# Optimization experiments

Measured on AMD Instinct MI355X. Metric: run time of the kernel, lower is better.

## Reference

```python
import jax, jax.numpy as jnp
import numpy as np

EMB = 8
HID = 64
B = 1000
T = 512
N = (B * T) // 5  # events per source; sources partition the (batch,time) grid

_KEYS = ["ccba", "cdtx", "cust", "dp", "remit"]
_NUMS = {"ccba": 8, "cdtx": 1, "cust": 1, "dp": 2, "remit": 1}
_CATS = {"ccba": 0, "cdtx": 2, "cust": 3, "dp": 8, "remit": 1}
_VOCAB = {"ccba": 0, "cdtx": 179, "cust": 37, "dp": 435, "remit": 5}


def setup_inputs() -> dict:
    ks = iter(jax.random.split(jax.random.key(0), 64))
    rng = np.random.default_rng(0)
    chunks = np.split(rng.permutation(B * T), 5)
    d = {}
    for k5, ch in zip(_KEYS, chunks):
        d[k5 + "_num"] = jax.random.normal(next(ks), (N, _NUMS[k5]), jnp.float32)
        if _CATS[k5] > 0:
            d[k5 + "_cat"] = jax.random.randint(next(ks), (N, _CATS[k5]), 0, _VOCAB[k5])
            d[k5 + "_tab"] = jax.random.normal(next(ks), (_VOCAB[k5], EMB), jnp.float32) * 0.1
        d[k5 + "_bi"] = jnp.asarray(ch // T, jnp.int32)
        d[k5 + "_ti"] = jnp.asarray(ch % T, jnp.int32)
        in_dim = _CATS[k5] * EMB + _NUMS[k5]
        d[k5 + "_W"] = jax.random.normal(next(ks), (in_dim, HID), jnp.float32) * np.float32(1.0 / np.sqrt(in_dim))
        d[k5 + "_b"] = jnp.zeros((HID,), jnp.float32)
    # LSTM: 2 layers x 2 directions, hidden 64, proj_size 1 -> layer1 input is 2
    for l, insz in [(0, HID), (1, 2)]:
        d[f"Wih{l}"] = jax.random.normal(next(ks), (2, 4 * HID, insz), jnp.float32) * 0.05
        d[f"Whh{l}"] = jax.random.normal(next(ks), (2, 4 * HID, 1), jnp.float32) * 0.05
        d[f"Whr{l}"] = jax.random.normal(next(ks), (2, 1, HID), jnp.float32) * 0.05
        d[f"bih{l}"] = jnp.zeros((2, 4 * HID), jnp.float32)
        d[f"bhh{l}"] = jnp.zeros((2, 4 * HID), jnp.float32)
    d["length"] = T
    d["batch_size"] = B
    return d


def _embed(num, cat, tab, W, b):
    # FeatureEmbedder: concat(categorical embeddings, numeric) -> Linear(hidden)
    x = num if cat is None else jnp.concatenate([tab[cat].reshape(cat.shape[0], -1), num], axis=-1)
    return x @ W + b


def _lstm_dir(x, Wih, Whh, Whr, bih, bhh, reverse):
    Bx = x.shape[0]
    H = Whr.shape[1]
    p = Whr.shape[0]
    bias = bih + bhh

    def step(carry, xt):
        h, c = carry  # h: [B,p] projected hidden, c: [B,H] cell
        g = xt @ Wih.T + h @ Whh.T + bias
        i, f, gg, o = jnp.split(g, 4, axis=-1)  # PyTorch gate order i,f,g,o
        c = jax.nn.sigmoid(f) * c + jax.nn.sigmoid(i) * jnp.tanh(gg)
        h = (jax.nn.sigmoid(o) * jnp.tanh(c)) @ Whr.T  # proj_size projection
        return (h, c), h

    init = (jnp.zeros((Bx, p), x.dtype), jnp.zeros((Bx, H), x.dtype))
    _, ys = jax.lax.scan(step, init, jnp.swapaxes(x, 0, 1), reverse=reverse)
    return jnp.swapaxes(ys, 0, 1)  # [B,T,p]


def _bilstm(x, Wih, Whh, Whr, bih, bhh):
    fwd = _lstm_dir(x, Wih[0], Whh[0], Whr[0], bih[0], bhh[0], False)
    bwd = _lstm_dir(x, Wih[1], Whh[1], Whr[1], bih[1], bhh[1], True)
    return jnp.concatenate([fwd, bwd], axis=-1)


def _forward(a):
    feat = jnp.zeros((a["batch_size"], a["length"], HID), jnp.float32)
    for k5 in _KEYS:
        v = _embed(a[k5 + "_num"], a.get(k5 + "_cat"), a.get(k5 + "_tab"), a[k5 + "_W"], a[k5 + "_b"])
        feat = feat.at[a[k5 + "_bi"], a[k5 + "_ti"]].set(v)  # scatter-assemble padded tensor
    h = _bilstm(feat, a["Wih0"], a["Whh0"], a["Whr0"], a["bih0"], a["bhh0"])
    h = _bilstm(h, a["Wih1"], a["Whh1"], a["Whr1"], a["bih1"], a["bhh1"])
    return h.mean(axis=2)  # [B,T]


def reference(ccba_num, ccba_bi, ccba_ti, ccba_W, ccba_b,
              cdtx_num, cdtx_cat, cdtx_tab, cdtx_bi, cdtx_ti, cdtx_W, cdtx_b,
              cust_num, cust_cat, cust_tab, cust_bi, cust_ti, cust_W, cust_b,
              dp_num, dp_cat, dp_tab, dp_bi, dp_ti, dp_W, dp_b,
              remit_num, remit_cat, remit_tab, remit_bi, remit_ti, remit_W, remit_b,
              Wih0, Whh0, Whr0, bih0, bhh0, Wih1, Whh1, Whr1, bih1, bhh1,
              length, batch_size):
    return _forward(dict(locals()))
```

## Files before the change

### kernel.cpp

```cpp
#include <hip/hip_runtime.h>
#include <cstdint>
#include <cstddef>

#define TLEN 512
#define BATCH 1000
#define NEVS 102400
#define HID 64
#define W0S 8
#define NP (TLEN / W0S)

__device__ __forceinline__ float fast_rcp(float x) {
#if __has_builtin(__builtin_amdgcn_rcpf)
    return __builtin_amdgcn_rcpf(x);
#else
    return 1.0f / x;
#endif
}
__device__ __forceinline__ float sigm(float x) { return fast_rcp(1.0f + __expf(-x)); }
__device__ __forceinline__ float tanh_f(float x) { return fmaf(2.0f, sigm(2.0f * x), -1.0f); }

__device__ __forceinline__ float wave_sum_bcast(float x) {
#if __has_builtin(__builtin_amdgcn_update_dpp) && __has_builtin(__builtin_amdgcn_readlane)
    x += __int_as_float(__builtin_amdgcn_update_dpp(0, __float_as_int(x), 0x111, 0xf, 0xf, true));
    x += __int_as_float(__builtin_amdgcn_update_dpp(0, __float_as_int(x), 0x112, 0xf, 0xf, true));
    x += __int_as_float(__builtin_amdgcn_update_dpp(0, __float_as_int(x), 0x114, 0xf, 0xf, true));
    x += __int_as_float(__builtin_amdgcn_update_dpp(0, __float_as_int(x), 0x118, 0xf, 0xf, true));
    x += __int_as_float(__builtin_amdgcn_update_dpp(0, __float_as_int(x), 0x142, 0xa, 0xf, true));
    x += __int_as_float(__builtin_amdgcn_update_dpp(0, __float_as_int(x), 0x143, 0xc, 0xf, true));
    return __int_as_float(__builtin_amdgcn_readlane(__float_as_int(x), 63));
#else
#pragma unroll
    for (int off = 1; off < 64; off <<= 1) x += __shfl_xor(x, off, 64);
    return x;
#endif
}

__device__ __forceinline__ void wave_sum2(float& a, float& b) {
#if __has_builtin(__builtin_amdgcn_update_dpp) && __has_builtin(__builtin_amdgcn_readlane)
    int ta, tb;
    ta = __builtin_amdgcn_update_dpp(0, __float_as_int(a), 0x111, 0xf, 0xf, true);
    tb = __builtin_amdgcn_update_dpp(0, __float_as_int(b), 0x111, 0xf, 0xf, true);
    a += __int_as_float(ta); b += __int_as_float(tb);
    ta = __builtin_amdgcn_update_dpp(0, __float_as_int(a), 0x112, 0xf, 0xf, true);
    tb = __builtin_amdgcn_update_dpp(0, __float_as_int(b), 0x112, 0xf, 0xf, true);
    a += __int_as_float(ta); b += __int_as_float(tb);
    ta = __builtin_amdgcn_update_dpp(0, __float_as_int(a), 0x114, 0xf, 0xf, true);
    tb = __builtin_amdgcn_update_dpp(0, __float_as_int(b), 0x114, 0xf, 0xf, true);
    a += __int_as_float(ta); b += __int_as_float(tb);
    ta = __builtin_amdgcn_update_dpp(0, __float_as_int(a), 0x118, 0xf, 0xf, true);
    tb = __builtin_amdgcn_update_dpp(0, __float_as_int(b), 0x118, 0xf, 0xf, true);
    a += __int_as_float(ta); b += __int_as_float(tb);
    ta = __builtin_amdgcn_update_dpp(0, __float_as_int(a), 0x142, 0xa, 0xf, true);
    tb = __builtin_amdgcn_update_dpp(0, __float_as_int(b), 0x142, 0xa, 0xf, true);
    a += __int_as_float(ta); b += __int_as_float(tb);
    ta = __builtin_amdgcn_update_dpp(0, __float_as_int(a), 0x143, 0xc, 0xf, true);
    tb = __builtin_amdgcn_update_dpp(0, __float_as_int(b), 0x143, 0xc, 0xf, true);
    a += __int_as_float(ta); b += __int_as_float(tb);
    a = __int_as_float(__builtin_amdgcn_readlane(__float_as_int(a), 63));
    b = __int_as_float(__builtin_amdgcn_readlane(__float_as_int(b), 63));
#else
    a = wave_sum_bcast(a); b = wave_sum_bcast(b);
#endif
}

__global__ __launch_bounds__(256) void map_build_kernel(
    const int* __restrict__ b0, const int* __restrict__ t0,
    const int* __restrict__ b1, const int* __restrict__ t1,
    const int* __restrict__ b2, const int* __restrict__ t2,
    const int* __restrict__ b3, const int* __restrict__ t3,
    const int* __restrict__ b4, const int* __restrict__ t4,
    int* __restrict__ map)
{
    const int src = blockIdx.y;
    const int* bi = src == 0 ? b0 : src == 1 ? b1 : src == 2 ? b2 : src == 3 ? b3 : b4;
    const int* ti = src == 0 ? t0 : src == 1 ? t1 : src == 2 ? t2 : src == 3 ? t3 : t4;
    const int e = blockIdx.x * 256 + threadIdx.x;
    map[bi[e] * TLEN + ti[e]] = (src << 20) | e;
}

__global__ __launch_bounds__(512) void compose_kernel(
    const float* __restrict__ W0, const float* __restrict__ B0,
    const float* __restrict__ W1, const float* __restrict__ B1,
    const float* __restrict__ W2, const float* __restrict__ B2,
    const float* __restrict__ W3, const float* __restrict__ B3,
    const float* __restrict__ W4, const float* __restrict__ B4,
    const float* __restrict__ Wih, const float* __restrict__ bih,
    const float* __restrict__ bhh, float* __restrict__ wp)
{
    const int col = threadIdx.x;
    const int row = blockIdx.x;
    const float* srcW; const float* srcB; int base, IND;
    if (row < 9)        { srcW = W0; srcB = B0; base = 0;   IND = 8;  }
    else if (row < 27)  { srcW = W1; srcB = B1; base = 9;   IND = 17; }
    else if (row < 53)  { srcW = W2; srcB = B2; base = 27;  IND = 25; }
    else if (row < 120) { srcW = W3; srcB = B3; base = 53;  IND = 66; }
    else                { srcW = W4; srcB = B4; base = 120; IND = 9;  }
    const int j = row - base;
    const float* xrow = (j < IND) ? (srcW + (size_t)j * 64) : srcB;
    const float* wr = Wih + (size_t)col * 64;
    float acc = 0.0f;
#pragma unroll
    for (int h2 = 0; h2 < 64; ++h2) acc = fmaf(xrow[h2], wr[h2], acc);
    if (j == IND) acc += bih[col] + bhh[col];
    wp[(size_t)row * 512 + col] = acc;
}

template<int NB, int BASE>
__device__ __forceinline__ float4 dot4(const float* wT, const float* xb, int colq) {
    float ax = 0.f, ay = 0.f, az = 0.f, aw = 0.f;
#pragma unroll
    for (int jb = 0; jb < NB; ++jb) {
        const float4 x4 = *(const float4*)(xb + 4 * jb);
        const float* w = wT + (size_t)(BASE + 4 * jb) * 256 + 4 * colq;
        const float4 w0 = *(const float4*)(w);
        const float4 w1 = *(const float4*)(w + 256);
        const float4 w2 = *(const float4*)(w + 512);
        const float4 w3 = *(const float4*)(w + 768);
        ax = fmaf(x4.x, w0.x, ax); ay = fmaf(x4.x, w0.y, ay);
        az = fmaf(x4.x, w0.z, az); aw = fmaf(x4.x, w0.w, aw);
        ax = fmaf(x4.y, w1.x, ax); ay = fmaf(x4.y, w1.y, ay);
        az = fmaf(x4.y, w1.z, az); aw = fmaf(x4.y, w1.w, aw);
        ax = fmaf(x4.z, w2.x, ax); ay = fmaf(x4.z, w2.y, ay);
        az = fmaf(x4.z, w2.z, az); aw = fmaf(x4.z, w2.w, aw);
        ax = fmaf(x4.w, w3.x, ax); ay = fmaf(x4.w, w3.y, ay);
        az = fmaf(x4.w, w3.z, az); aw = fmaf(x4.w, w3.w, aw);
    }
    return make_float4(ax, ay, az, aw);
}

__global__ __launch_bounds__(576, 1) void fused0_kernel(
    const float* __restrict__ ccba_num,
    const float* __restrict__ cdtx_num, const int* __restrict__ cdtx_cat, const float* __restrict__ cdtx_tab,
    const float* __restrict__ cust_num, const int* __restrict__ cust_cat, const float* __restrict__ cust_tab,
    const float* __restrict__ dp_num,   const int* __restrict__ dp_cat,   const float* __restrict__ dp_tab,
    const float* __restrict__ remit_num, const int* __restrict__ remit_cat, const float* __restrict__ remit_tab,
    const float* __restrict__ wp, const int* __restrict__ map,
    const float* __restrict__ Whh, const float* __restrict__ Whr,
    float* __restrict__ h0)
{
    __shared__ float wT[132 * 256];
    __shared__ float winP[2][W0S][256];
    __shared__ float xbuf[2][W0S][68];
    __shared__ int   mcls[2][W0S];

    const int tid = threadIdx.x;
    const int b = blockIdx.x >> 1, dir = blockIdx.x & 1;

    {
        const float4* wp4 = (const float4*)wp;
        float4* wT4 = (float4*)wT;
        for (int i = tid; i < 130 * 64; i += 576) {
            const int row = i >> 6, c4 = i & 63;
            wT4[(row << 6) + c4] = wp4[(row << 7) + (dir << 6) + c4];
        }
        if (tid < 128) wT4[130 * 64 + tid] = make_float4(0.f, 0.f, 0.f, 0.f);
    }

    float whh4[4] = {0.f, 0.f, 0.f, 0.f};
    float whr = 0.f, h = 0.f, c = 0.f;
    float* h0p = h0 + (size_t)b * TLEN * 2 + dir;
    if (tid >= 512) {
        const int lane = tid - 512;
#pragma unroll
        for (int k = 0; k < 4; ++k) whh4[k] = Whh[dir * 256 + k * 64 + lane];
        whr = Whr[dir * HID + lane];
    }

    struct GR { float v0, v1; int mc; };

    auto g_load = [&](int P) -> GR {
        GR g; g.v0 = 0.f; g.v1 = 0.f;
        const int ev = tid >> 6, v = tid & 63;
        const int s = P * W0S + ev;
        const int t = dir ? (TLEN - 1 - s) : s;
        g.mc = map[b * TLEN + t];
        const int src = g.mc >> 20, e = g.mc & 0xFFFFF;
        switch (src) {
        case 0:
            g.v0 = (v < 8) ? ccba_num[(size_t)e * 8 + v] : (v == 8 ? 1.0f : 0.0f);
            break;
        case 1:
            g.v0 = (v < 16) ? cdtx_tab[(size_t)cdtx_cat[e * 2 + (v >> 3)] * 8 + (v & 7)]
                 : (v == 16 ? cdtx_num[e] : (v == 17 ? 1.0f : 0.0f));
            break;
        case 2:
            g.v0 = (v < 24) ? cust_tab[(size_t)cust_cat[e * 3 + (v >> 3)] * 8 + (v & 7)]
                 : (v == 24 ? cust_num[e] : (v == 25 ? 1.0f : 0.0f));
            break;
        case 3:
            g.v0 = dp_tab[(size_t)dp_cat[e * 8 + (v >> 3)] * 8 + (v & 7)];
            if (v < 4) g.v1 = (v < 2) ? dp_num[(size_t)e * 2 + v] : (v == 2 ? 1.0f : 0.0f);
            break;
        default:
            g.v0 = (v < 8) ? remit_tab[(size_t)remit_cat[e] * 8 + v]
                 : (v == 8 ? remit_num[e] : (v == 9 ? 1.0f : 0.0f));
            break;
        }
        return g;
    };
    auto g_store = [&](const GR& g, int P) {
        const int buf = P & 1;
        const int ev = tid >> 6, v = tid & 63;
        if (v == 0) mcls[buf][ev] = g.mc;
        const int src = g.mc >> 20;
        const int pad = (src == 0) ? 12 : (src == 1) ? 20 : (src == 2) ? 28
                      : (src == 3) ? 64 : 12;
        if (v < pad) xbuf[buf][ev][v] = g.v0;
        if (src == 3 && v < 4) xbuf[buf][ev][64 + v] = g.v1;
    };

    auto a1 = [&](int P) {
        const int buf = P & 1;
        const int ev = tid >> 6, colq = tid & 63;
        const int src = mcls[buf][ev] >> 20;
        const float* xb = xbuf[buf][ev];
        float4 acc;
        switch (src) {
        case 0:  acc = dot4<3, 0>(wT, xb, colq);   break;
        case 1:  acc = dot4<5, 9>(wT, xb, colq);   break;
        case 2:  acc = dot4<7, 27>(wT, xb, colq);  break;
        case 3:  acc = dot4<17, 53>(wT, xb, colq); break;
        default: acc = dot4<3, 120>(wT, xb, colq); break;
        }
        ((float4*)winP[buf][ev])[colq] = acc;
    };

    auto bstep = [&](int P) {
        const int buf = P & 1;
        const int lane = tid - 512;
        for (int sl = 0; sl < W0S; ++sl) {
            const float gi = fmaf(whh4[0], h, winP[buf][sl][lane]);
            const float gf = fmaf(whh4[1], h, winP[buf][sl][64 + lane]);
            const float gg = fmaf(whh4[2], h, winP[buf][sl][128 + lane]);
            const float go = fmaf(whh4[3], h, winP[buf][sl][192 + lane]);
            c = sigm(gf) * c + sigm(gi) * tanh_f(gg);
            h = wave_sum_bcast(sigm(go) * tanh_f(c) * whr);
            const int s = P * W0S + sl;
            const int tt = dir ? (TLEN - 1 - s) : s;
            if (lane == 0) h0p[(size_t)tt * 2] = h;
        }
    };

    if (tid < 512) { GR g0 = g_load(0); g_store(g0, 0); }
    __syncthreads();
    if (tid < 512) { GR g1 = g_load(1); a1(0); g_store(g1, 1); }
    __syncthreads();

    for (int p = 0; p < NP; ++p) {
        if (tid < 512) {
            GR g{};
            const bool hg = (p + 2 < NP);
            if (hg) g = g_load(p + 2);
            if (p + 1 < NP) a1(p + 1);
            if (hg) g_store(g, p + 2);
        } else if (tid < 576) {
            bstep(p);
        }
        __syncthreads();
    }
}

__global__ __launch_bounds__(256, 2) void lstm1_kernel(
    const float* __restrict__ h0, const float* __restrict__ Wih,
    const float* __restrict__ Whh, const float* __restrict__ Whr,
    const float* __restrict__ bih, const float* __restrict__ bhh,
    float* __restrict__ h1)
{
    const int w = threadIdx.x >> 6, lane = threadIdx.x & 63;
    const int b = blockIdx.x * 4 + w;

    const volatile float* vWih = Wih;
    const volatile float* vWhh = Whh;
    const volatile float* vWhr = Whr;
    const volatile float* vbih = bih;
    const volatile float* vbhh = bhh;

    float wi0[2][4], wi1[2][4], whh[2][4], bias[2][4], whr[2];
#pragma unroll
    for (int d = 0; d < 2; ++d) {
#pragma unroll
        for (int k = 0; k < 4; ++k) {
            const int r = d * 256 + k * 64 + lane;
            wi0[d][k] = vWih[(size_t)r * 2 + 0];
            wi1[d][k] = vWih[(size_t)r * 2 + 1];
            whh[d][k] = vWhh[r];
            bias[d][k] = vbih[r] + vbhh[r];
        }
        whr[d] = vWhr[d * HID + lane];
    }
    float hA = 0, cA = 0, hB = 0, cB = 0;
    const float* hb = h0 + (size_t)b * TLEN * 2;

    float2 xA = *(const float2*)(hb);
    float2 xB = *(const float2*)(hb + (size_t)(TLEN - 1) * 2);
    for (int t = 0; t < TLEN; ++t) {
        const int tn = (t + 1 < TLEN) ? t + 1 : t;
        const float2 xAn = *(const float2*)(hb + (size_t)tn * 2);
        const float2 xBn = *(const float2*)(hb + (size_t)(TLEN - 1 - tn) * 2);
        float gA[4], gB[4];
#pragma unroll
        for (int k = 0; k < 4; ++k) {
            gA[k] = fmaf(whh[0][k], hA, fmaf(wi1[0][k], xA.y, fmaf(wi0[0][k], xA.x, bias[0][k])));
            gB[k] = fmaf(whh[1][k], hB, fmaf(wi1[1][k], xB.y, fmaf(wi0[1][k], xB.x, bias[1][k])));
        }
        cA = sigm(gA[1]) * cA + sigm(gA[0]) * tanh_f(gA[2]);
        cB = sigm(gB[1]) * cB + sigm(gB[0]) * tanh_f(gB[2]);
        float pA = sigm(gA[3]) * tanh_f(cA) * whr[0];
        float pB = sigm(gB[3]) * tanh_f(cB) * whr[1];
        wave_sum2(pA, pB);
        hA = pA; hB = pB;
        if (lane == 0) {
            h1[((size_t)b * TLEN + t) * 2 + 0] = hA;
            h1[((size_t)b * TLEN + (TLEN - 1 - t)) * 2 + 1] = hB;
        }
        xA = xAn; xB = xBn;
    }
}

__global__ __launch_bounds__(256) void mean_kernel(
    const float2* __restrict__ h1, float* __restrict__ out)
{
    int i = blockIdx.x * 256 + threadIdx.x;
    if (i < BATCH * TLEN) {
        float2 v = h1[i];
        out[i] = 0.5f * (v.x + v.y);
    }
}

extern "C" void kernel_launch(void* const* d_in, const int* in_sizes, int n_in,
                              void* d_out, int out_size, void* d_ws, size_t ws_size,
                              hipStream_t stream)
{
    const float* ccba_num = (const float*)d_in[0];
    const int*   ccba_bi  = (const int*)d_in[1];
    const int*   ccba_ti  = (const int*)d_in[2];
    const float* ccba_W   = (const float*)d_in[3];
    const float* ccba_b   = (const float*)d_in[4];
    const float* cdtx_num = (const float*)d_in[5];
    const int*   cdtx_cat = (const int*)d_in[6];
    const float* cdtx_tab = (const float*)d_in[7];
    const int*   cdtx_bi  = (const int*)d_in[8];
    const int*   cdtx_ti  = (const int*)d_in[9];
    const float* cdtx_W   = (const float*)d_in[10];
    const float* cdtx_b   = (const float*)d_in[11];
    const float* cust_num = (const float*)d_in[12];
    const int*   cust_cat = (const int*)d_in[13];
    const float* cust_tab = (const float*)d_in[14];
    const int*   cust_bi  = (const int*)d_in[15];
    const int*   cust_ti  = (const int*)d_in[16];
    const float* cust_W   = (const float*)d_in[17];
    const float* cust_b   = (const float*)d_in[18];
    const float* dp_num   = (const float*)d_in[19];
    const int*   dp_cat   = (const int*)d_in[20];
    const float* dp_tab   = (const float*)d_in[21];
    const int*   dp_bi    = (const int*)d_in[22];
    const int*   dp_ti    = (const int*)d_in[23];
    const float* dp_W     = (const float*)d_in[24];
    const float* dp_b     = (const float*)d_in[25];
    const float* remit_num = (const float*)d_in[26];
    const int*   remit_cat = (const int*)d_in[27];
    const float* remit_tab = (const float*)d_in[28];
    const int*   remit_bi  = (const int*)d_in[29];
    const int*   remit_ti  = (const int*)d_in[30];
    const float* remit_W   = (const float*)d_in[31];
    const float* remit_b   = (const float*)d_in[32];
    const float* Wih0 = (const float*)d_in[33];
    const float* Whh0 = (const float*)d_in[34];
    const float* Whr0 = (const float*)d_in[35];
    const float* bih0 = (const float*)d_in[36];
    const float* bhh0 = (const float*)d_in[37];
    const float* Wih1 = (const float*)d_in[38];
    const float* Whh1 = (const float*)d_in[39];
    const float* Whr1 = (const float*)d_in[40];
    const float* bih1 = (const float*)d_in[41];
    const float* bhh1 = (const float*)d_in[42];

    float* out = (float*)d_out;

    char* ws = (char*)d_ws;
    float* wp  = (float*)ws;
    int*   map = (int*)  (ws + 266240ull);
    float* h0  = (float*)(ws + 266240ull + 2048000ull);
    float* h1  = (float*)(ws + 266240ull + 2048000ull + 4096000ull);

    compose_kernel<<<130, 512, 0, stream>>>(
        ccba_W, ccba_b, cdtx_W, cdtx_b, cust_W, cust_b,
        dp_W, dp_b, remit_W, remit_b, Wih0, bih0, bhh0, wp);

    map_build_kernel<<<dim3(NEVS / 256, 5), 256, 0, stream>>>(
        ccba_bi, ccba_ti, cdtx_bi, cdtx_ti, cust_bi, cust_ti,
        dp_bi, dp_ti, remit_bi, remit_ti, map);

    fused0_kernel<<<2 * BATCH, 576, 0, stream>>>(
        ccba_num,
        cdtx_num, cdtx_cat, cdtx_tab,
        cust_num, cust_cat, cust_tab,
        dp_num, dp_cat, dp_tab,
        remit_num, remit_cat, remit_tab,
        wp, map, Whh0, Whr0, h0);

    lstm1_kernel<<<250, 256, 0, stream>>>(h0, Wih1, Whh1, Whr1, bih1, bhh1, h1);
    mean_kernel<<<(BATCH * TLEN + 255) / 256, 256, 0, stream>>>((const float2*)h1, out);
}
```

Baseline: 1.459 ms.

## Split layer-0 LSTM into chunked batched projection and recurrence kernels

Replaces the fused per-sequence kernel, which interleaved gather, input projection and recurrence inside one block per (batch, direction), with a time-chunked loop of two kernels. A persistent projection kernel buckets 64 positions by source and computes gate pre-activations four events at a time against shared-memory weights, writing them to a global buffer. A recurrence kernel runs one sequence per wave over each chunk, carrying h and c state across launches. The aim is better weight reuse and occupancy for the projection, and a lighter recurrence kernel, at the cost of global round trips for gate values, extra launches, and a chunk size that depends on workspace size.

```diff
diff --git a/kernel.cpp b/kernel.cpp
--- a/kernel.cpp
+++ b/kernel.cpp
@@ -6,8 +6,6 @@
 #define BATCH 1000
 #define NEVS 102400
 #define HID 64
-#define W0S 8
-#define NP (TLEN / W0S)
 
 __device__ __forceinline__ float fast_rcp(float x) {
 #if __has_builtin(__builtin_amdgcn_rcpf)
@@ -106,158 +104,230 @@
 }
 
 template<int NB, int BASE>
-__device__ __forceinline__ float4 dot4(const float* wT, const float* xb, int colq) {
-    float ax = 0.f, ay = 0.f, az = 0.f, aw = 0.f;
+__device__ __forceinline__ void run_group(
+    const float* __restrict__ wT, const float (*xb)[68],
+    const int li[4], const bool val[4], const int pv[4],
+    float* __restrict__ gdst, int lane)
+{
+    float acc[4][4] = {{0.f, 0.f, 0.f, 0.f}, {0.f, 0.f, 0.f, 0.f},
+                       {0.f, 0.f, 0.f, 0.f}, {0.f, 0.f, 0.f, 0.f}};
 #pragma unroll
     for (int jb = 0; jb < NB; ++jb) {
-        const float4 x4 = *(const float4*)(xb + 4 * jb);
-        const float* w = wT + (size_t)(BASE + 4 * jb) * 256 + 4 * colq;
+        float4 xk[4];
+#pragma unroll
+        for (int k = 0; k < 4; ++k) xk[k] = *(const float4*)&xb[li[k]][4 * jb];
+        const float* w = wT + (size_t)(BASE + 4 * jb) * 256 + 4 * lane;
         const float4 w0 = *(const float4*)(w);
         const float4 w1 = *(const float4*)(w + 256);
         const float4 w2 = *(const float4*)(w + 512);
         const float4 w3 = *(const float4*)(w + 768);
-        ax = fmaf(x4.x, w0.x, ax); ay = fmaf(x4.x, w0.y, ay);
-        az = fmaf(x4.x, w0.z, az); aw = fmaf(x4.x, w0.w, aw);
-        ax = fmaf(x4.y, w1.x, ax); ay = fmaf(x4.y, w1.y, ay);
-        az = fmaf(x4.y, w1.z, az); aw = fmaf(x4.y, w1.w, aw);
-        ax = fmaf(x4.z, w2.x, ax); ay = fmaf(x4.z, w2.y, ay);
-        az = fmaf(x4.z, w2.z, az); aw = fmaf(x4.z, w2.w, aw);
-        ax = fmaf(x4.w, w3.x, ax); ay = fmaf(x4.w, w3.y, ay);
-        az = fmaf(x4.w, w3.z, az); aw = fmaf(x4.w, w3.w, aw);
-    }
-    return make_float4(ax, ay, az, aw);
-}
-
-__global__ __launch_bounds__(576, 1) void fused0_kernel(
+#pragma unroll
+        for (int k = 0; k < 4; ++k) {
+            acc[k][0] = fmaf(xk[k].x, w0.x, acc[k][0]);
+            acc[k][1] = fmaf(xk[k].x, w0.y, acc[k][1]);
+            acc[k][2] = fmaf(xk[k].x, w0.z, acc[k][2]);
+            acc[k][3] = fmaf(xk[k].x, w0.w, acc[k][3]);
+            acc[k][0] = fmaf(xk[k].y, w1.x, acc[k][0]);
+            acc[k][1] = fmaf(xk[k].y, w1.y, acc[k][1]);
+            acc[k][2] = fmaf(xk[k].y, w1.z, acc[k][2]);
+            acc[k][3] = fmaf(xk[k].y, w1.w, acc[k][3]);
+            acc[k][0] = fmaf(xk[k].z, w2.x, acc[k][0]);
+            acc[k][1] = fmaf(xk[k].z, w2.y, acc[k][1]);
+            acc[k][2] = fmaf(xk[k].z, w2.z, acc[k][2]);
+            acc[k][3] = fmaf(xk[k].z, w2.w, acc[k][3]);
+            acc[k][0] = fmaf(xk[k].w, w3.x, acc[k][0]);
+            acc[k][1] = fmaf(xk[k].w, w3.y, acc[k][1]);
+            acc[k][2] = fmaf(xk[k].w, w3.z, acc[k][2]);
+            acc[k][3] = fmaf(xk[k].w, w3.w, acc[k][3]);
+        }
+    }
+#pragma unroll
+    for (int k = 0; k < 4; ++k)
+        if (val[k])
+            *(float4*)(gdst + (size_t)pv[k] * 256 + 4 * lane) =
+                make_float4(acc[k][0], acc[k][1], acc[k][2], acc[k][3]);
+}
+
+__global__ __launch_bounds__(512, 1) void project_kernel(
     const float* __restrict__ ccba_num,
     const float* __restrict__ cdtx_num, const int* __restrict__ cdtx_cat, const float* __restrict__ cdtx_tab,
     const float* __restrict__ cust_num, const int* __restrict__ cust_cat, const float* __restrict__ cust_tab,
     const float* __restrict__ dp_num,   const int* __restrict__ dp_cat,   const float* __restrict__ dp_tab,
     const float* __restrict__ remit_num, const int* __restrict__ remit_cat, const float* __restrict__ remit_tab,
     const float* __restrict__ wp, const int* __restrict__ map,
-    const float* __restrict__ Whh, const float* __restrict__ Whr,
-    float* __restrict__ h0)
+    float* __restrict__ gf, float* __restrict__ gb,
+    int f0, int len, int tcm)
 {
     __shared__ float wT[132 * 256];
-    __shared__ float winP[2][W0S][256];
-    __shared__ float xbuf[2][W0S][68];
-    __shared__ int   mcls[2][W0S];
+    __shared__ float xbuf[64][68];
+    __shared__ int ev_e[64], ev_src[64], ev_pos[64];
+    __shared__ int lists[5][64];
+    __shared__ int cnt[5];
+    __shared__ int glist[96];
+    __shared__ int ng;
 
     const int tid = threadIdx.x;
-    const int b = blockIdx.x >> 1, dir = blockIdx.x & 1;
+    const int dir = blockIdx.y;
+    const int lane = tid & 63, wave = tid >> 6;
+    float* gdst = dir ? gb : gf;
 
     {
         const float4* wp4 = (const float4*)wp;
         float4* wT4 = (float4*)wT;
-        for (int i = tid; i < 130 * 64; i += 576) {
+        for (int i = tid; i < 132 * 64; i += 512) {
             const int row = i >> 6, c4 = i & 63;
-            wT4[(row << 6) + c4] = wp4[(row << 7) + (dir << 6) + c4];
-        }
-        if (tid < 128) wT4[130 * 64 + tid] = make_float4(0.f, 0.f, 0.f, 0.f);
-    }
-
-    float whh4[4] = {0.f, 0.f, 0.f, 0.f};
-    float whr = 0.f, h = 0.f, c = 0.f;
+            wT4[i] = (row < 130) ? wp4[(row << 7) + (dir << 6) + c4]
+                                 : make_float4(0.f, 0.f, 0.f, 0.f);
+        }
+    }
+    __syncthreads();
+
+    const int npos = 1000 * len;
+    const int ntiles = (npos + 63) >> 6;
+
+    for (int tile = blockIdx.x; tile < ntiles; tile += gridDim.x) {
+        if (tid < 5) cnt[tid] = 0;
+        __syncthreads();
+
+        if (tid < 64) {
+            const int idx = (tile << 6) + tid;
+            int srcv = 0;
+            if (idx < npos) {
+                const int b = idx / len, lt = idx - b * len;
+                const int t = dir ? (TLEN - 1 - f0 - lt) : (f0 + lt);
+                const int mc = map[b * TLEN + t];
+                srcv = mc >> 20;
+                ev_e[tid] = mc & 0xFFFFF;
+                ev_pos[tid] = b * tcm + lt;
+                const int slot = atomicAdd(&cnt[srcv], 1);
+                lists[srcv][slot] = tid;
+            } else {
+                ev_e[tid] = 0;
+            }
+            ev_src[tid] = srcv;
+        }
+        __syncthreads();
+
+        if (tid == 0) {
+            int g = 0;
+            for (int s = 0; s < 5; ++s)
+                for (int base = 0; base < cnt[s]; base += 4)
+                    glist[g++] = (s << 8) | base;
+            ng = g;
+        }
+        for (int r = 0; r < 64; r += 8) {
+            const int i = r + wave;
+            const int e = ev_e[i];
+            const int s = ev_src[i];
+            const int v = lane;
+            float v0;
+            switch (s) {
+            case 0:
+                v0 = (v < 8) ? ccba_num[(size_t)e * 8 + v] : (v == 8 ? 1.f : 0.f);
+                if (v < 12) xbuf[i][v] = v0;
+                break;
+            case 1:
+                v0 = (v < 16) ? cdtx_tab[(size_t)cdtx_cat[e * 2 + (v >> 3)] * 8 + (v & 7)]
+                   : (v == 16 ? cdtx_num[e] : (v == 17 ? 1.f : 0.f));
+                if (v < 20) xbuf[i][v] = v0;
+                break;
+            case 2:
+                v0 = (v < 24) ? cust_tab[(size_t)cust_cat[e * 3 + (v >> 3)] * 8 + (v & 7)]
+                   : (v == 24 ? cust_num[e] : (v == 25 ? 1.f : 0.f));
+                if (v < 28) xbuf[i][v] = v0;
+                break;
+            case 3:
+                xbuf[i][v] = dp_tab[(size_t)dp_cat[e * 8 + (v >> 3)] * 8 + (v & 7)];
+                if (v < 4) xbuf[i][64 + v] = (v < 2) ? dp_num[(size_t)e * 2 + v]
+                                                     : (v == 2 ? 1.f : 0.f);
+                break;
+            default:
+                v0 = (v < 8) ? remit_tab[(size_t)remit_cat[e] * 8 + v]
+                   : (v == 8 ? remit_num[e] : (v == 9 ? 1.f : 0.f));
+                if (v < 12) xbuf[i][v] = v0;
+                break;
+            }
+        }
+        __syncthreads();
+
+        for (int gi = wave; gi < ng; gi += 8) {
+            const int s = glist[gi] >> 8, base = glist[gi] & 255;
+            const int n = cnt[s];
+            int li[4]; bool val[4]; int pv[4];
+#pragma unroll
+            for (int k = 0; k < 4; ++k) {
+                const int j = base + k;
+                val[k] = j < n;
+                li[k] = lists[s][val[k] ? j : base];
+                pv[k] = ev_pos[li[k]];
+            }
+            switch (s) {
+            case 0:  run_group<3, 0>(wT, xbuf, li, val, pv, gdst, lane);   break;
+            case 1:  run_group<5, 9>(wT, xbuf, li, val, pv, gdst, lane);   break;
+            case 2:  run_group<7, 27>(wT, xbuf, li, val, pv, gdst, lane);  break;
+            case 3:  run_group<17, 53>(wT, xbuf, li, val, pv, gdst, lane); break;
+            default: run_group<3, 120>(wT, xbuf, li, val, pv, gdst, lane); break;
+            }
+        }
+        __syncthreads();
+    }
+}
+
+__global__ __launch_bounds__(256) void rec_chunk_kernel(
+    const float* __restrict__ gf, const float* __restrict__ gb,
+    const float* __restrict__ Whh, const float* __restrict__ Whr,
+    float* __restrict__ h0, float* __restrict__ hs, float* __restrict__ cs,
+    int f0, int len, int tcm, int first)
+{
+    const int wv = threadIdx.x >> 6, lane = threadIdx.x & 63;
+    const int p = blockIdx.x * 4 + wv;
+    const int b = p >> 1, dir = p & 1;
+
+    float whh4[4];
+#pragma unroll
+    for (int k = 0; k < 4; ++k) whh4[k] = Whh[dir * 256 + k * 64 + lane];
+    const float whr = Whr[dir * HID + lane];
+
+    const float* g = (dir ? gb : gf) + (size_t)b * tcm * 256 + lane;
     float* h0p = h0 + (size_t)b * TLEN * 2 + dir;
-    if (tid >= 512) {
-        const int lane = tid - 512;
-#pragma unroll
-        for (int k = 0; k < 4; ++k) whh4[k] = Whh[dir * 256 + k * 64 + lane];
-        whr = Whr[dir * HID + lane];
-    }
-
-    struct GR { float v0, v1; int mc; };
-
-    auto g_load = [&](int P) -> GR {
-        GR g; g.v0 = 0.f; g.v1 = 0.f;
-        const int ev = tid >> 6, v = tid & 63;
-        const int s = P * W0S + ev;
-        const int t = dir ? (TLEN - 1 - s) : s;
-        g.mc = map[b * TLEN + t];
-        const int src = g.mc >> 20, e = g.mc & 0xFFFFF;
-        switch (src) {
-        case 0:
-            g.v0 = (v < 8) ? ccba_num[(size_t)e * 8 + v] : (v == 8 ? 1.0f : 0.0f);
-            break;
-        case 1:
-            g.v0 = (v < 16) ? cdtx_tab[(size_t)cdtx_cat[e * 2 + (v >> 3)] * 8 + (v & 7)]
-                 : (v == 16 ? cdtx_num[e] : (v == 17 ? 1.0f : 0.0f));
-            break;
-        case 2:
-            g.v0 = (v < 24) ? cust_tab[(size_t)cust_cat[e * 3 + (v >> 3)] * 8 + (v & 7)]
-                 : (v == 24 ? cust_num[e] : (v == 25 ? 1.0f : 0.0f));
-            break;
-        case 3:
-            g.v0 = dp_tab[(size_t)dp_cat[e * 8 + (v >> 3)] * 8 + (v & 7)];
-            if (v < 4) g.v1 = (v < 2) ? dp_num[(size_t)e * 2 + v] : (v == 2 ? 1.0f : 0.0f);
-            break;
-        default:
-            g.v0 = (v < 8) ? remit_tab[(size_t)remit_cat[e] * 8 + v]
-                 : (v == 8 ? remit_num[e] : (v == 9 ? 1.0f : 0.0f));
-            break;
-        }
-        return g;
+
+    float h, c;
+    if (first) { h = 0.0f; c = 0.0f; }
+    else       { h = hs[p]; c = cs[(size_t)p * 64 + lane]; }
+
+    auto ga = [&](int s) -> const float* {
+        const int sc = (s < len) ? s : (len - 1);
+        return g + (size_t)sc * 256;
     };
-    auto g_store = [&](const GR& g, int P) {
-        const int buf = P & 1;
-        const int ev = tid >> 6, v = tid & 63;
-        if (v == 0) mcls[buf][ev] = g.mc;
-        const int src = g.mc >> 20;
-        const int pad = (src == 0) ? 12 : (src == 1) ? 20 : (src == 2) ? 28
-                      : (src == 3) ? 64 : 12;
-        if (v < pad) xbuf[buf][ev][v] = g.v0;
-        if (src == 3 && v < 4) xbuf[buf][ev][64 + v] = g.v1;
+    auto do_step = [&](const float (&G)[4], int s) {
+        const float gi = fmaf(whh4[0], h, G[0]);
+        const float gfv = fmaf(whh4[1], h, G[1]);
+        const float gg = fmaf(whh4[2], h, G[2]);
+        const float go = fmaf(whh4[3], h, G[3]);
+        c = sigm(gfv) * c + sigm(gi) * tanh_f(gg);
+        h = wave_sum_bcast(sigm(go) * tanh_f(c) * whr);
+        const int t_out = dir ? (TLEN - 1 - f0 - s) : (f0 + s);
+        if (lane == 0) h0p[(size_t)t_out * 2] = h;
     };
 
-    auto a1 = [&](int P) {
-        const int buf = P & 1;
-        const int ev = tid >> 6, colq = tid & 63;
-        const int src = mcls[buf][ev] >> 20;
-        const float* xb = xbuf[buf][ev];
-        float4 acc;
-        switch (src) {
-        case 0:  acc = dot4<3, 0>(wT, xb, colq);   break;
-        case 1:  acc = dot4<5, 9>(wT, xb, colq);   break;
-        case 2:  acc = dot4<7, 27>(wT, xb, colq);  break;
-        case 3:  acc = dot4<17, 53>(wT, xb, colq); break;
-        default: acc = dot4<3, 120>(wT, xb, colq); break;
-        }
-        ((float4*)winP[buf][ev])[colq] = acc;
-    };
-
-    auto bstep = [&](int P) {
-        const int buf = P & 1;
-        const int lane = tid - 512;
-        for (int sl = 0; sl < W0S; ++sl) {
-            const float gi = fmaf(whh4[0], h, winP[buf][sl][lane]);
-            const float gf = fmaf(whh4[1], h, winP[buf][sl][64 + lane]);
-            const float gg = fmaf(whh4[2], h, winP[buf][sl][128 + lane]);
-            const float go = fmaf(whh4[3], h, winP[buf][sl][192 + lane]);
-            c = sigm(gf) * c + sigm(gi) * tanh_f(gg);
-            h = wave_sum_bcast(sigm(go) * tanh_f(c) * whr);
-            const int s = P * W0S + sl;
-            const int tt = dir ? (TLEN - 1 - s) : s;
-            if (lane == 0) h0p[(size_t)tt * 2] = h;
-        }
-    };
-
-    if (tid < 512) { GR g0 = g_load(0); g_store(g0, 0); }
-    __syncthreads();
-    if (tid < 512) { GR g1 = g_load(1); a1(0); g_store(g1, 1); }
-    __syncthreads();
-
-    for (int p = 0; p < NP; ++p) {
-        if (tid < 512) {
-            GR g{};
-            const bool hg = (p + 2 < NP);
-            if (hg) g = g_load(p + 2);
-            if (p + 1 < NP) a1(p + 1);
-            if (hg) g_store(g, p + 2);
-        } else if (tid < 576) {
-            bstep(p);
-        }
-        __syncthreads();
-    }
+    float A[4], B[4];
+    {
+        const float* pa = ga(0); const float* pb = ga(1);
+#pragma unroll
+        for (int k = 0; k < 4; ++k) { A[k] = pa[k * 64]; B[k] = pb[k * 64]; }
+    }
+    for (int s = 0; s < len; s += 2) {
+        float C[4], D[4];
+        const float* pc = ga(s + 2); const float* pd = ga(s + 3);
+#pragma unroll
+        for (int k = 0; k < 4; ++k) { C[k] = pc[k * 64]; D[k] = pd[k * 64]; }
+        do_step(A, s);
+        if (s + 1 < len) do_step(B, s + 1);
+#pragma unroll
+        for (int k = 0; k < 4; ++k) { A[k] = C[k]; B[k] = D[k]; }
+    }
+    if (lane == 0) hs[p] = h;
+    cs[(size_t)p * 64 + lane] = c;
 }
 
 __global__ __launch_bounds__(256, 2) void lstm1_kernel(
@@ -377,11 +447,25 @@
 
     float* out = (float*)d_out;
 
+    const size_t FIXED = 2048000ull + 4096000ull + 4096000ull + 266240ull
+                       + 8000ull + 512000ull;
+    size_t avail = (ws_size > FIXED) ? (ws_size - FIXED) : 0;
+    int tcm = (int)(avail / 2048000ull);
+    if (tcm < 1) tcm = 1;
+    if (tcm > 86) tcm = 86;
+    if (tcm >= 2) tcm &= ~1;
+
     char* ws = (char*)d_ws;
-    float* wp  = (float*)ws;
-    int*   map = (int*)  (ws + 266240ull);
-    float* h0  = (float*)(ws + 266240ull + 2048000ull);
-    float* h1  = (float*)(ws + 266240ull + 2048000ull + 4096000ull);
+    const size_t gfB = (size_t)tcm * 1024000ull;
+    float* gf    = (float*)ws;
+    float* gb    = (float*)(ws + gfB);
+    char*  fixed = ws + 2 * gfB;
+    int*   map   = (int*)  fixed;
+    float* h0    = (float*)(fixed + 2048000ull);
+    float* h1    = (float*)(fixed + 2048000ull + 4096000ull);
+    float* wp    = (float*)(fixed + 2048000ull + 8192000ull);
+    float* hs    = (float*)(fixed + 2048000ull + 8192000ull + 266240ull);
+    float* cs    = (float*)(fixed + 2048000ull + 8192000ull + 266240ull + 8000ull);
 
     compose_kernel<<<130, 512, 0, stream>>>(
         ccba_W, ccba_b, cdtx_W, cdtx_b, cust_W, cust_b,
@@ -391,13 +475,20 @@
         ccba_bi, ccba_ti, cdtx_bi, cdtx_ti, cust_bi, cust_ti,
         dp_bi, dp_ti, remit_bi, remit_ti, map);
 
-    fused0_kernel<<<2 * BATCH, 576, 0, stream>>>(
-        ccba_num,
-        cdtx_num, cdtx_cat, cdtx_tab,
-        cust_num, cust_cat, cust_tab,
-        dp_num, dp_cat, dp_tab,
-        remit_num, remit_cat, remit_tab,
-        wp, map, Whh0, Whr0, h0);
+    int first = 1;
+    for (int f0 = 0; f0 < TLEN; f0 += tcm) {
+        const int len = (TLEN - f0 < tcm) ? (TLEN - f0) : tcm;
+        project_kernel<<<dim3(128, 2), 512, 0, stream>>>(
+            ccba_num,
+            cdtx_num, cdtx_cat, cdtx_tab,
+            cust_num, cust_cat, cust_tab,
+            dp_num, dp_cat, dp_tab,
+            remit_num, remit_cat, remit_tab,
+            wp, map, gf, gb, f0, len, tcm);
+        rec_chunk_kernel<<<500, 256, 0, stream>>>(
+            gf, gb, Whh0, Whr0, h0, hs, cs, f0, len, tcm, first);
+        first = 0;
+    }
 
     lstm1_kernel<<<250, 256, 0, stream>>>(h0, Wih1, Whh1, Whr1, bih1, bhh1, h1);
     mean_kernel<<<(BATCH * TLEN + 255) / 256, 256, 0, stream>>>((const float2*)h1, out);
```

Measured after the change: 4.639 ms. 218% more time.

## Batch eight sequences per block with source-grouped paired input projections

Applied to the files above, without the earlier changes.

The fused layer-0 kernel now runs one 1024-thread block per direction for each group of eight batch rows, instead of one block per (batch, direction). Eight waves each run the LSTM recurrence for one sequence, two timesteps per phase. The other waves gather features and compute input projections. The 16 events of each phase are grouped by source type, so each wave computes two events of the same source and reuses each weight load from shared memory. This amortizes the per-block weight staging and reduces wasted gate compute, at the cost of two barriers per two timesteps and only 250 blocks, which may leave CUs underused.

```diff
diff --git a/kernel.cpp b/kernel.cpp
--- a/kernel.cpp
+++ b/kernel.cpp
@@ -6,8 +6,6 @@
 #define BATCH 1000
 #define NEVS 102400
 #define HID 64
-#define W0S 8
-#define NP (TLEN / W0S)
 
 __device__ __forceinline__ float fast_rcp(float x) {
 #if __has_builtin(__builtin_amdgcn_rcpf)
@@ -105,30 +103,31 @@
     wp[(size_t)row * 512 + col] = acc;
 }
 
-template<int NB, int BASE>
-__device__ __forceinline__ float4 dot4(const float* wT, const float* xb, int colq) {
-    float ax = 0.f, ay = 0.f, az = 0.f, aw = 0.f;
-#pragma unroll
-    for (int jb = 0; jb < NB; ++jb) {
-        const float4 x4 = *(const float4*)(xb + 4 * jb);
-        const float* w = wT + (size_t)(BASE + 4 * jb) * 256 + 4 * colq;
+__device__ __forceinline__ void fma4(float4& a, float x, const float4 w) {
+    a.x = fmaf(x, w.x, a.x); a.y = fmaf(x, w.y, a.y);
+    a.z = fmaf(x, w.z, a.z); a.w = fmaf(x, w.w, a.w);
+}
+
+template<int NG, int BASE>
+__device__ __forceinline__ void dot_pair(
+    const float* __restrict__ wT, const float* __restrict__ xb0,
+    const float* __restrict__ xb1, float4& a0, float4& a1, int lane)
+{
+#pragma unroll
+    for (int g = 0; g < NG; ++g) {
+        const float4 x0 = *(const float4*)(xb0 + 4 * g);
+        const float4 x1 = *(const float4*)(xb1 + 4 * g);
+        const float* w = wT + (size_t)(BASE + 4 * g) * 256 + 4 * lane;
         const float4 w0 = *(const float4*)(w);
         const float4 w1 = *(const float4*)(w + 256);
         const float4 w2 = *(const float4*)(w + 512);
         const float4 w3 = *(const float4*)(w + 768);
-        ax = fmaf(x4.x, w0.x, ax); ay = fmaf(x4.x, w0.y, ay);
-        az = fmaf(x4.x, w0.z, az); aw = fmaf(x4.x, w0.w, aw);
-        ax = fmaf(x4.y, w1.x, ax); ay = fmaf(x4.y, w1.y, ay);
-        az = fmaf(x4.y, w1.z, az); aw = fmaf(x4.y, w1.w, aw);
-        ax = fmaf(x4.z, w2.x, ax); ay = fmaf(x4.z, w2.y, ay);
-        az = fmaf(x4.z, w2.z, az); aw = fmaf(x4.z, w2.w, aw);
-        ax = fmaf(x4.w, w3.x, ax); ay = fmaf(x4.w, w3.y, ay);
-        az = fmaf(x4.w, w3.z, az); aw = fmaf(x4.w, w3.w, aw);
-    }
-    return make_float4(ax, ay, az, aw);
-}
-
-__global__ __launch_bounds__(576, 1) void fused0_kernel(
+        fma4(a0, x0.x, w0); fma4(a0, x0.y, w1); fma4(a0, x0.z, w2); fma4(a0, x0.w, w3);
+        fma4(a1, x1.x, w0); fma4(a1, x1.y, w1); fma4(a1, x1.z, w2); fma4(a1, x1.w, w3);
+    }
+}
+
+__global__ __launch_bounds__(1024, 1) void fused0_kernel(
     const float* __restrict__ ccba_num,
     const float* __restrict__ cdtx_num, const int* __restrict__ cdtx_cat, const float* __restrict__ cdtx_tab,
     const float* __restrict__ cust_num, const int* __restrict__ cust_cat, const float* __restrict__ cust_tab,
@@ -139,122 +138,162 @@
     float* __restrict__ h0)
 {
     __shared__ float wT[132 * 256];
-    __shared__ float winP[2][W0S][256];
-    __shared__ float xbuf[2][W0S][68];
-    __shared__ int   mcls[2][W0S];
+    __shared__ float winP[8][2][256];
+    __shared__ float xsh[2][16][72];
+    __shared__ int   srcs[2][16];
 
     const int tid = threadIdx.x;
-    const int b = blockIdx.x >> 1, dir = blockIdx.x & 1;
+    const int wave = tid >> 6, lane = tid & 63;
+    const int dir = blockIdx.y;
+    const int b0g = blockIdx.x * 8;
 
     {
         const float4* wp4 = (const float4*)wp;
         float4* wT4 = (float4*)wT;
-        for (int i = tid; i < 130 * 64; i += 576) {
+        for (int i = tid; i < 132 * 64; i += 1024) {
             const int row = i >> 6, c4 = i & 63;
-            wT4[(row << 6) + c4] = wp4[(row << 7) + (dir << 6) + c4];
-        }
-        if (tid < 128) wT4[130 * 64 + tid] = make_float4(0.f, 0.f, 0.f, 0.f);
+            wT4[i] = (row < 130) ? wp4[(row << 7) + (dir << 6) + c4]
+                                 : make_float4(0.f, 0.f, 0.f, 0.f);
+        }
     }
 
     float whh4[4] = {0.f, 0.f, 0.f, 0.f};
     float whr = 0.f, h = 0.f, c = 0.f;
-    float* h0p = h0 + (size_t)b * TLEN * 2 + dir;
-    if (tid >= 512) {
-        const int lane = tid - 512;
+    float* h0p = nullptr;
+    if (wave < 8) {
 #pragma unroll
         for (int k = 0; k < 4; ++k) whh4[k] = Whh[dir * 256 + k * 64 + lane];
         whr = Whr[dir * HID + lane];
-    }
-
-    struct GR { float v0, v1; int mc; };
-
-    auto g_load = [&](int P) -> GR {
-        GR g; g.v0 = 0.f; g.v1 = 0.f;
-        const int ev = tid >> 6, v = tid & 63;
-        const int s = P * W0S + ev;
-        const int t = dir ? (TLEN - 1 - s) : s;
-        g.mc = map[b * TLEN + t];
-        const int src = g.mc >> 20, e = g.mc & 0xFFFFF;
-        switch (src) {
-        case 0:
-            g.v0 = (v < 8) ? ccba_num[(size_t)e * 8 + v] : (v == 8 ? 1.0f : 0.0f);
-            break;
-        case 1:
-            g.v0 = (v < 16) ? cdtx_tab[(size_t)cdtx_cat[e * 2 + (v >> 3)] * 8 + (v & 7)]
-                 : (v == 16 ? cdtx_num[e] : (v == 17 ? 1.0f : 0.0f));
-            break;
-        case 2:
-            g.v0 = (v < 24) ? cust_tab[(size_t)cust_cat[e * 3 + (v >> 3)] * 8 + (v & 7)]
-                 : (v == 24 ? cust_num[e] : (v == 25 ? 1.0f : 0.0f));
-            break;
-        case 3:
-            g.v0 = dp_tab[(size_t)dp_cat[e * 8 + (v >> 3)] * 8 + (v & 7)];
-            if (v < 4) g.v1 = (v < 2) ? dp_num[(size_t)e * 2 + v] : (v == 2 ? 1.0f : 0.0f);
-            break;
-        default:
-            g.v0 = (v < 8) ? remit_tab[(size_t)remit_cat[e] * 8 + v]
-                 : (v == 8 ? remit_num[e] : (v == 9 ? 1.0f : 0.0f));
-            break;
-        }
-        return g;
+        h0p = h0 + (size_t)(b0g + wave) * TLEN * 2 + dir;
+    }
+
+    auto gather = [&](int pp) {
+        const int nbuf = pp & 1;
+        const int gi = wave - 8;
+#pragma unroll
+        for (int q = 0; q < 2; ++q) {
+            const int ev = gi * 2 + q;
+            const int bl = ev >> 1, sl = ev & 1;
+            const int s = 2 * pp + sl;
+            const int t = dir ? (TLEN - 1 - s) : s;
+            const int mc = map[(b0g + bl) * TLEN + t];
+            const int src = mc >> 20, e = mc & 0xFFFFF;
+            const int v = lane;
+            if (v == 0) srcs[nbuf][ev] = src;
+            float* xb = xsh[nbuf][ev];
+            switch (src) {
+            case 0:
+                if (v < 12) xb[v] = (v < 8) ? ccba_num[(size_t)e * 8 + v]
+                                            : (v == 8 ? 1.f : 0.f);
+                break;
+            case 1:
+                if (v < 20) xb[v] = (v < 16) ? cdtx_tab[(size_t)cdtx_cat[e * 2 + (v >> 3)] * 8 + (v & 7)]
+                                  : (v == 16 ? cdtx_num[e] : (v == 17 ? 1.f : 0.f));
+                break;
+            case 2:
+                if (v < 28) xb[v] = (v < 24) ? cust_tab[(size_t)cust_cat[e * 3 + (v >> 3)] * 8 + (v & 7)]
+                                  : (v == 24 ? cust_num[e] : (v == 25 ? 1.f : 0.f));
+                break;
+            case 3:
+                xb[v] = dp_tab[(size_t)dp_cat[e * 8 + (v >> 3)] * 8 + (v & 7)];
+                if (v < 4) xb[64 + v] = (v < 2) ? dp_num[(size_t)e * 2 + v]
+                                                : (v == 2 ? 1.f : 0.f);
+                break;
+            default:
+                if (v < 12) xb[v] = (v < 8) ? remit_tab[(size_t)remit_cat[e] * 8 + v]
+                                  : (v == 8 ? remit_num[e] : (v == 9 ? 1.f : 0.f));
+                break;
+            }
+        }
     };
-    auto g_store = [&](const GR& g, int P) {
-        const int buf = P & 1;
-        const int ev = tid >> 6, v = tid & 63;
-        if (v == 0) mcls[buf][ev] = g.mc;
-        const int src = g.mc >> 20;
-        const int pad = (src == 0) ? 12 : (src == 1) ? 20 : (src == 2) ? 28
-                      : (src == 3) ? 64 : 12;
-        if (v < pad) xbuf[buf][ev][v] = g.v0;
-        if (src == 3 && v < 4) xbuf[buf][ev][64 + v] = g.v1;
-    };
-
-    auto a1 = [&](int P) {
-        const int buf = P & 1;
-        const int ev = tid >> 6, colq = tid & 63;
-        const int src = mcls[buf][ev] >> 20;
-        const float* xb = xbuf[buf][ev];
-        float4 acc;
-        switch (src) {
-        case 0:  acc = dot4<3, 0>(wT, xb, colq);   break;
-        case 1:  acc = dot4<5, 9>(wT, xb, colq);   break;
-        case 2:  acc = dot4<7, 27>(wT, xb, colq);  break;
-        case 3:  acc = dot4<17, 53>(wT, xb, colq); break;
-        default: acc = dot4<3, 120>(wT, xb, colq); break;
-        }
-        ((float4*)winP[buf][ev])[colq] = acc;
-    };
-
-    auto bstep = [&](int P) {
-        const int buf = P & 1;
-        const int lane = tid - 512;
-        for (int sl = 0; sl < W0S; ++sl) {
-            const float gi = fmaf(whh4[0], h, winP[buf][sl][lane]);
-            const float gf = fmaf(whh4[1], h, winP[buf][sl][64 + lane]);
-            const float gg = fmaf(whh4[2], h, winP[buf][sl][128 + lane]);
-            const float go = fmaf(whh4[3], h, winP[buf][sl][192 + lane]);
-            c = sigm(gf) * c + sigm(gi) * tanh_f(gg);
-            h = wave_sum_bcast(sigm(go) * tanh_f(c) * whr);
-            const int s = P * W0S + sl;
-            const int tt = dir ? (TLEN - 1 - s) : s;
-            if (lane == 0) h0p[(size_t)tt * 2] = h;
-        }
-    };
-
-    if (tid < 512) { GR g0 = g_load(0); g_store(g0, 0); }
+
+    if (wave >= 8) gather(0);
     __syncthreads();
-    if (tid < 512) { GR g1 = g_load(1); a1(0); g_store(g1, 1); }
-    __syncthreads();
-
-    for (int p = 0; p < NP; ++p) {
-        if (tid < 512) {
-            GR g{};
-            const bool hg = (p + 2 < NP);
-            if (hg) g = g_load(p + 2);
-            if (p + 1 < NP) a1(p + 1);
-            if (hg) g_store(g, p + 2);
-        } else if (tid < 576) {
-            bstep(p);
+
+    const int NPH = TLEN / 2;
+    for (int p = 0; p < NPH; ++p) {
+        const int buf = p & 1;
+
+        {
+            unsigned m0 = 0, m1 = 0, m2 = 0, m3 = 0, m4 = 0;
+#pragma unroll
+            for (int ev = 0; ev < 16; ++ev) {
+                const int s = srcs[buf][ev];
+                const unsigned bit = 1u << ev;
+                m0 |= (s == 0) ? bit : 0u;
+                m1 |= (s == 1) ? bit : 0u;
+                m2 |= (s == 2) ? bit : 0u;
+                m3 |= (s == 3) ? bit : 0u;
+                m4 |= (s == 4) ? bit : 0u;
+            }
+            int rem = wave, src = -1, ev0 = 0, ev1 = 0, pair = 0;
+#pragma unroll
+            for (int s = 0; s < 5; ++s) {
+                const unsigned m = (s == 0) ? m0 : (s == 1) ? m1 : (s == 2) ? m2
+                                 : (s == 3) ? m3 : m4;
+                const int gs = (__popc(m) + 1) >> 1;
+                if (src < 0) {
+                    if (rem < gs) {
+                        unsigned mm = m;
+                        for (int k = 0; k < rem; ++k) { mm &= mm - 1; mm &= mm - 1; }
+                        ev0 = __ffs(mm) - 1; mm &= mm - 1;
+                        pair = (mm != 0);
+                        ev1 = pair ? (__ffs(mm) - 1) : ev0;
+                        src = s;
+                    } else {
+                        rem -= gs;
+                    }
+                }
+            }
+            if (src >= 0) {
+                const float* xb0 = xsh[buf][ev0];
+                const float* xb1 = xsh[buf][ev1];
+                float4 a0 = make_float4(0.f, 0.f, 0.f, 0.f);
+                float4 a1 = make_float4(0.f, 0.f, 0.f, 0.f);
+                switch (src) {
+                case 0:  dot_pair<3, 0>(wT, xb0, xb1, a0, a1, lane);   break;
+                case 1:  dot_pair<5, 9>(wT, xb0, xb1, a0, a1, lane);   break;
+                case 2:  dot_pair<7, 27>(wT, xb0, xb1, a0, a1, lane);  break;
+                case 3:  dot_pair<17, 53>(wT, xb0, xb1, a0, a1, lane); break;
+                default: dot_pair<3, 120>(wT, xb0, xb1, a0, a1, lane); break;
+                }
+                ((float4*)&winP[ev0 >> 1][ev0 & 1][0])[lane] = a0;
+                if (pair) ((float4*)&winP[ev1 >> 1][ev1 & 1][0])[lane] = a1;
+            }
+        }
+        __syncthreads();
+
+        if (wave < 8) {
+            float G0[4], G1[4];
+#pragma unroll
+            for (int k = 0; k < 4; ++k) {
+                G0[k] = winP[wave][0][k * 64 + lane];
+                G1[k] = winP[wave][1][k * 64 + lane];
+            }
+            {
+                const float gi = fmaf(whh4[0], h, G0[0]);
+                const float gf = fmaf(whh4[1], h, G0[1]);
+                const float gg = fmaf(whh4[2], h, G0[2]);
+                const float go = fmaf(whh4[3], h, G0[3]);
+                c = sigm(gf) * c + sigm(gi) * tanh_f(gg);
+                h = wave_sum_bcast(sigm(go) * tanh_f(c) * whr);
+                const int s = 2 * p;
+                const int t = dir ? (TLEN - 1 - s) : s;
+                if (lane == 0) h0p[(size_t)t * 2] = h;
+            }
+            {
+                const float gi = fmaf(whh4[0], h, G1[0]);
+                const float gf = fmaf(whh4[1], h, G1[1]);
+                const float gg = fmaf(whh4[2], h, G1[2]);
+                const float go = fmaf(whh4[3], h, G1[3]);
+                c = sigm(gf) * c + sigm(gi) * tanh_f(gg);
+                h = wave_sum_bcast(sigm(go) * tanh_f(c) * whr);
+                const int s = 2 * p + 1;
+                const int t = dir ? (TLEN - 1 - s) : s;
+                if (lane == 0) h0p[(size_t)t * 2] = h;
+            }
+        } else if (p + 1 < NPH) {
+            gather(p + 1);
         }
         __syncthreads();
     }
@@ -391,7 +430,7 @@
         ccba_bi, ccba_ti, cdtx_bi, cdtx_ti, cust_bi, cust_ti,
         dp_bi, dp_ti, remit_bi, remit_ti, map);
 
-    fused0_kernel<<<2 * BATCH, 576, 0, stream>>>(
+    fused0_kernel<<<dim3(BATCH / 8, 2), 1024, 0, stream>>>(
         ccba_num,
         cdtx_num, cdtx_cat, cdtx_tab,
         cust_num, cust_cat, cust_tab,
```

New measurement: 1.521 ms. 1.04x slower.
